# Optimization experiments

Measured on AMD Instinct MI355X. Metric: run time of the kernel, lower is better.

Reference implementation:

```python
import jax, jax.numpy as jnp
import numpy as np

B, N, E = 4, 50000, 800000
C_IN, C_OUT, K = 64, 64, 3  # K = max_degree
AVG_DEG = 16.0


def setup_inputs() -> dict:
    key = jax.random.key(0)
    k1, k2, k3, k4, k5 = jax.random.split(key, 5)
    x = jax.random.normal(k1, (B, N, C_IN), dtype=jnp.float32)
    lap_rows = jax.random.randint(k2, (E,), 0, N)
    lap_cols = jax.random.randint(k3, (E,), 0, N)
    # scale so ||L|| stays O(1) and the Chebyshev recursion is stable
    lap_vals = jax.random.normal(k4, (E,), dtype=jnp.float32) / AVG_DEG
    weights = jax.random.normal(k5, (K + 1, C_IN, C_OUT), dtype=jnp.float32) * 0.1
    bias = jnp.full((C_OUT,), 0.1, dtype=jnp.float32)
    return dict(x=x, lap_rows=lap_rows, lap_cols=lap_cols,
                lap_vals=lap_vals, weights=weights, bias=bias)


def reference(x, lap_rows, lap_cols, lap_vals, weights, bias):
    # Sparse L @ X via edge list: gather source rows, scale, scatter-add to dest rows.
    def spmm_one(xb):  # xb: [N, C]
        return jax.ops.segment_sum(lap_vals[:, None] * xb[lap_cols], lap_rows,
                                   num_segments=N)

    spmm = jax.vmap(spmm_one)  # [B, N, C] -> [B, N, C]

    Tx0 = x
    out = jnp.einsum('bnc,co->bno', Tx0, weights[0])
    Tx1 = spmm(Tx0)
    out = out + jnp.einsum('bnc,co->bno', Tx1, weights[1])
    for k in range(2, K + 1):
        Tx2 = 2.0 * spmm(Tx1) - Tx0
        out = out + jnp.einsum('bnc,co->bno', Tx2, weights[k])
        Tx0, Tx1 = Tx1, Tx2
    return jax.nn.relu(out + bias)
```

## Files before the change

### kernel.cpp

```cpp
#include <hip/hip_runtime.h>


#define N_NODES 50000
#define N_EDGES 800000
#define BATCH 4
#define CH 64
#define BN (N_NODES * CH)
#define ROWS_TOTAL (BATCH * N_NODES)
#define NB 782
#define EPB 4096
#define SCT_BLOCKS ((N_EDGES + EPB - 1) / EPB)

typedef unsigned int uint;
typedef unsigned short ushort;
typedef unsigned char uchar;
typedef __attribute__((ext_vector_type(8))) short short8;
typedef __attribute__((ext_vector_type(4))) float f32x4;

__device__ __forceinline__ uint pack_bf16(float lo, float hi) {
  uint a = __float_as_uint(lo);
  uint b = __float_as_uint(hi);
  a = (a + 0x7fffu + ((a >> 16) & 1u)) >> 16;
  b = (b + 0x7fffu + ((b >> 16) & 1u)) >> 16;
  return a | (b << 16);
}
__device__ __forceinline__ ushort bf16one(float x) {
  uint a = __float_as_uint(x);
  a = (a + 0x7fffu + ((a >> 16) & 1u)) >> 16;
  return (ushort)a;
}
__device__ __forceinline__ uint q_u8(float v, float inv) {
  return (uint)((int)rintf(v * inv) + 128) & 0xffu;
}

__global__ __launch_bounds__(1024) void bucket_hist(const int* __restrict__ rows,
                                                    int* __restrict__ gcounts) {
  __shared__ int h[NB];
  for (int b = threadIdx.x; b < NB; b += 1024) h[b] = 0;
  __syncthreads();
  int base_e = blockIdx.x * EPB;
#pragma unroll
  for (int j = 0; j < EPB / 1024; ++j) {
    int e = base_e + j * 1024 + threadIdx.x;
    if (e < N_EDGES) atomicAdd(&h[rows[e] >> 6], 1);
  }
  __syncthreads();
  for (int b = threadIdx.x; b < NB; b += 1024)
    if (h[b]) atomicAdd(&gcounts[b], h[b]);
}

__global__ __launch_bounds__(1024) void bucket_scan(const int* __restrict__ gcounts,
                                                    int* __restrict__ bucket_base,
                                                    int* __restrict__ gcursor) {
  __shared__ int s[1024];
  int t = threadIdx.x;
  int v = (t < NB) ? gcounts[t] : 0;
  s[t] = v;
  __syncthreads();
  for (int off = 1; off < 1024; off <<= 1) {
    int tv = (t >= off) ? s[t - off] : 0;
    __syncthreads();
    s[t] += tv;
    __syncthreads();
  }
  int ex = s[t] - v;
  if (t < NB) { bucket_base[t] = ex; gcursor[t] = ex; }
  if (t == NB) bucket_base[NB] = N_EDGES;
}

__global__ __launch_bounds__(1024) void bucket_scatter(const int* __restrict__ rows,
                                                       const int* __restrict__ cols,
                                                       const float* __restrict__ vals,
                                                       int* __restrict__ gcursor,
                                                       uint2* __restrict__ staging) {
  __shared__ int lcur[NB];
  for (int b = threadIdx.x; b < NB; b += 1024) lcur[b] = 0;
  __syncthreads();
  int base_e = blockIdx.x * EPB;
#pragma unroll
  for (int j = 0; j < EPB / 1024; ++j) {
    int e = base_e + j * 1024 + threadIdx.x;
    if (e < N_EDGES) atomicAdd(&lcur[rows[e] >> 6], 1);
  }
  __syncthreads();
  for (int b = threadIdx.x; b < NB; b += 1024) {
    int c = lcur[b];
    lcur[b] = (c > 0) ? atomicAdd(&gcursor[b], c) : 0;
  }
  __syncthreads();
#pragma unroll
  for (int j = 0; j < EPB / 1024; ++j) {
    int e = base_e + j * 1024 + threadIdx.x;
    if (e < N_EDGES) {
      int r = rows[e];
      int pos = atomicAdd(&lcur[r >> 6], 1);
      staging[pos] = make_uint2((uint)cols[e] | ((uint)(r & 63) << 20),
                                __float_as_uint(vals[e]));
    }
  }
}

__global__ __launch_bounds__(256) void bucket_finalize(const int* __restrict__ bucket_base,
                                                       const uint2* __restrict__ staging,
                                                       uint2* __restrict__ pairs,
                                                       int* __restrict__ row_start) {
  int b = blockIdx.x;
  int seg0 = bucket_base[b], seg1 = bucket_base[b + 1];
  __shared__ int hist[64];
  __shared__ int cur[64];
  if (threadIdx.x < 64) hist[threadIdx.x] = 0;
  __syncthreads();
  for (int i = seg0 + threadIdx.x; i < seg1; i += 256)
    atomicAdd(&hist[staging[i].x >> 20], 1);
  __syncthreads();
  if (threadIdx.x < 64) {
    int v = hist[threadIdx.x];
    int sc = v;
#pragma unroll
    for (int off = 1; off < 64; off <<= 1) {
      int t = __shfl_up(sc, off, 64);
      if (threadIdx.x >= (unsigned)off) sc += t;
    }
    int start = seg0 + sc - v;
    cur[threadIdx.x] = start;
    int r = b * 64 + threadIdx.x;
    if (r < N_NODES) row_start[r] = start;
    if (r == N_NODES) row_start[N_NODES] = N_EDGES;
  }
  __syncthreads();
  for (int i = seg0 + threadIdx.x; i < seg1; i += 256) {
    uint2 eu = staging[i];
    int rl = eu.x >> 20;
    int pos = atomicAdd(&cur[rl], 1);
    pairs[pos] = make_uint2(eu.x & 0xFFFFFu, eu.y);
  }
}

__global__ __launch_bounds__(256) void wprep_kernel(const float* __restrict__ w,
                                                    ushort* __restrict__ wtT) {
  int t = blockIdx.x * 256 + threadIdx.x;
  if (t >= 64 * 256) return;
  int o = t >> 8, k = t & 255, m = k >> 6, c = k & 63;
  int idx = c * 64 + o;
  float v;
  if (m == 0)      v = w[idx] - w[2 * 4096 + idx];
  else if (m == 1) v = w[4096 + idx] - 3.0f * w[3 * 4096 + idx];
  else if (m == 2) v = 2.0f * w[2 * 4096 + idx];
  else             v = 4.0f * w[3 * 4096 + idx];
  wtT[t] = bf16one(v);
}

__global__ __launch_bounds__(256) void cvt_kernel(const float* __restrict__ in,
                                                  uint* __restrict__ xu8w,
                                                  float* __restrict__ xsc) {
  int node = blockIdx.x * 4 + (threadIdx.x >> 6);
  int lane = threadIdx.x & 63;
  int b = lane >> 4;
  int c4 = (lane & 15) * 4;
  float4 v = *reinterpret_cast<const float4*>(in + (size_t)b * BN + (size_t)node * 64 + c4);
  float mx = fmaxf(fmaxf(fabsf(v.x), fabsf(v.y)), fmaxf(fabsf(v.z), fabsf(v.w)));
#pragma unroll
  for (int off = 1; off < 64; off <<= 1) mx = fmaxf(mx, __shfl_xor(mx, off, 64));
  float inv = mx > 0.f ? 127.0f / mx : 0.f;
  uint w8 = q_u8(v.x, inv) | (q_u8(v.y, inv) << 8) |
            (q_u8(v.z, inv) << 16) | (q_u8(v.w, inv) << 24);
  xu8w[(size_t)node * 64 + b * 16 + (lane & 15)] = w8;
  if (lane == 0) xsc[node] = mx * (1.0f / 127.0f);
}

__device__ __forceinline__ void fma16_u8(float acc[16], float& sm, float m,
                                         const uint4& w) {
  const uint arr[4] = {w.x, w.y, w.z, w.w};
#pragma unroll
  for (int t = 0; t < 4; ++t) {
    uint u = arr[t];
    acc[t * 4 + 0] = fmaf(m, (float)(u & 0xffu),         acc[t * 4 + 0]);
    acc[t * 4 + 1] = fmaf(m, (float)((u >> 8) & 0xffu),  acc[t * 4 + 1]);
    acc[t * 4 + 2] = fmaf(m, (float)((u >> 16) & 0xffu), acc[t * 4 + 2]);
    acc[t * 4 + 3] = fmaf(m, (float)(u >> 24),           acc[t * 4 + 3]);
  }
  sm += m;
}

__device__ __forceinline__ void spmm_body(const int* __restrict__ row_start,
                                          const uint2* __restrict__ pairs,
                                          const uchar* __restrict__ src,
                                          const float* __restrict__ ssc,
                                          uchar* __restrict__ dst,
                                          float* __restrict__ dsc) {
  int row = blockIdx.x * 4 + (threadIdx.x >> 6);
  int lane = threadIdx.x & 63;
  int q = lane >> 4;
  int ql = lane & 15;
  const uchar* sb = src + ql * 16;
  int s = row_start[row], e = row_start[row + 1];
  float acc[16];
  float sm = 0.f;
#pragma unroll
  for (int j = 0; j < 16; ++j) acc[j] = 0.f;
  int i = s;
  for (; i + 15 < e; i += 16) {
    uint2 p0 = pairs[i + q];
    uint2 p1 = pairs[i + 4 + q];
    uint2 p2 = pairs[i + 8 + q];
    uint2 p3 = pairs[i + 12 + q];
    uint4 q0 = *reinterpret_cast<const uint4*>(sb + (size_t)p0.x * 256);
    uint4 q1 = *reinterpret_cast<const uint4*>(sb + (size_t)p1.x * 256);
    uint4 q2 = *reinterpret_cast<const uint4*>(sb + (size_t)p2.x * 256);
    uint4 q3 = *reinterpret_cast<const uint4*>(sb + (size_t)p3.x * 256);
    float m0 = __uint_as_float(p0.y) * ssc[p0.x];
    float m1 = __uint_as_float(p1.y) * ssc[p1.x];
    float m2 = __uint_as_float(p2.y) * ssc[p2.x];
    float m3 = __uint_as_float(p3.y) * ssc[p3.x];
    fma16_u8(acc, sm, m0, q0);
    fma16_u8(acc, sm, m1, q1);
    fma16_u8(acc, sm, m2, q2);
    fma16_u8(acc, sm, m3, q3);
  }
  for (; i < e; i += 4) {
    if (i + q < e) {
      uint2 p0 = pairs[i + q];
      uint4 q0 = *reinterpret_cast<const uint4*>(sb + (size_t)p0.x * 256);
      fma16_u8(acc, sm, __uint_as_float(p0.y) * ssc[p0.x], q0);
    }
  }
#pragma unroll
  for (int j = 0; j < 16; ++j) {
    acc[j] += __shfl_xor(acc[j], 16, 64);
    acc[j] += __shfl_xor(acc[j], 32, 64);
  }
  sm += __shfl_xor(sm, 16, 64);
  sm += __shfl_xor(sm, 32, 64);
#pragma unroll
  for (int j = 0; j < 16; ++j) acc[j] = fmaf(-128.f, sm, acc[j]);
  float mx = 0.f;
#pragma unroll
  for (int j = 0; j < 16; ++j) mx = fmaxf(mx, fabsf(acc[j]));
#pragma unroll
  for (int off = 1; off < 16; off <<= 1) mx = fmaxf(mx, __shfl_xor(mx, off, 64));
  if (lane < 16) {
    float inv = mx > 0.f ? 127.0f / mx : 0.f;
    uint w[4];
#pragma unroll
    for (int t = 0; t < 4; ++t) {
      w[t] = q_u8(acc[t * 4 + 0], inv) | (q_u8(acc[t * 4 + 1], inv) << 8) |
             (q_u8(acc[t * 4 + 2], inv) << 16) | (q_u8(acc[t * 4 + 3], inv) << 24);
    }
    *reinterpret_cast<uint4*>(dst + (size_t)row * 256 + ql * 16) =
        make_uint4(w[0], w[1], w[2], w[3]);
    if (lane == 0) dsc[row] = mx * (1.0f / 127.0f);
  }
}

__global__ __launch_bounds__(256) void spmm_s1(const int* __restrict__ rs,
                                               const uint2* __restrict__ pr,
                                               const uchar* __restrict__ src,
                                               const float* __restrict__ ssc,
                                               uchar* __restrict__ dst,
                                               float* __restrict__ dsc) {
  spmm_body(rs, pr, src, ssc, dst, dsc);
}
__global__ __launch_bounds__(256) void spmm_s2(const int* __restrict__ rs,
                                               const uint2* __restrict__ pr,
                                               const uchar* __restrict__ src,
                                               const float* __restrict__ ssc,
                                               uchar* __restrict__ dst,
                                               float* __restrict__ dsc) {
  spmm_body(rs, pr, src, ssc, dst, dsc);
}
__global__ __launch_bounds__(256) void spmm_s3(const int* __restrict__ rs,
                                               const uint2* __restrict__ pr,
                                               const uchar* __restrict__ src,
                                               const float* __restrict__ ssc,
                                               uchar* __restrict__ dst,
                                               float* __restrict__ dsc) {
  spmm_body(rs, pr, src, ssc, dst, dsc);
}

__device__ __forceinline__ short8 dequant8_u8(uint2 q, float sc, float nb) {
  float f0 = fmaf((float)(q.x & 0xffu),         sc, nb);
  float f1 = fmaf((float)((q.x >> 8) & 0xffu),  sc, nb);
  float f2 = fmaf((float)((q.x >> 16) & 0xffu), sc, nb);
  float f3 = fmaf((float)(q.x >> 24),           sc, nb);
  float f4 = fmaf((float)(q.y & 0xffu),         sc, nb);
  float f5 = fmaf((float)((q.y >> 8) & 0xffu),  sc, nb);
  float f6 = fmaf((float)((q.y >> 16) & 0xffu), sc, nb);
  float f7 = fmaf((float)(q.y >> 24),           sc, nb);
  uint4 v = make_uint4(pack_bf16(f0, f1), pack_bf16(f2, f3),
                       pack_bf16(f4, f5), pack_bf16(f6, f7));
  return __builtin_bit_cast(short8, v);
}

__global__ __launch_bounds__(256) void gemm4_mfma(
    const uchar* __restrict__ A0u8, const float* __restrict__ A0sc,
    const uchar* __restrict__ A1u8, const float* __restrict__ A1sc,
    const uchar* __restrict__ A2u8, const float* __restrict__ A2sc,
    const uchar* __restrict__ A3u8, const float* __restrict__ A3sc,
    const uint* __restrict__ wtT,
    const float* __restrict__ bias, float* __restrict__ out) {
  __shared__ uint WS[64 * 132];
  __shared__ float bias_s[64];
  for (int w = threadIdx.x; w < 8192; w += 256)
    WS[(w >> 7) * 132 + (w & 127)] = wtT[w];
  if (threadIdx.x < 64) bias_s[threadIdx.x] = bias[threadIdx.x];
  __syncthreads();

  const int lane = threadIdx.x & 63;
  const int wv = threadIdx.x >> 6;
  const int r0 = blockIdx.x * 64 + wv * 16;
  const int c16 = lane & 15;
  const int hi = lane >> 4;

  const int ar = r0 + c16;
  const size_t arow_b = (size_t)ar * 64 + hi * 8;
  const int nd = ar >> 2;
  const float sc0 = A0sc[nd];
  const float sc1 = A1sc[nd];
  const float sc2 = A2sc[nd];
  const float sc3 = A3sc[nd];

  f32x4 acc[4] = {{0.f, 0.f, 0.f, 0.f}, {0.f, 0.f, 0.f, 0.f},
                  {0.f, 0.f, 0.f, 0.f}, {0.f, 0.f, 0.f, 0.f}};

#pragma unroll
  for (int ks = 0; ks < 8; ++ks) {
    const int m = ks >> 1;
    const uchar* Au = (m == 0) ? A0u8 : (m == 1) ? A1u8 : (m == 2) ? A2u8 : A3u8;
    const float sc = (m == 0) ? sc0 : (m == 1) ? sc1 : (m == 2) ? sc2 : sc3;
    uint2 qv = *reinterpret_cast<const uint2*>(Au + arow_b + (ks & 1) * 32);
    short8 afrag = dequant8_u8(qv, sc, -128.f * sc);
#pragma unroll
    for (int nt = 0; nt < 4; ++nt) {
      uint4 bv = *reinterpret_cast<const uint4*>(
          &WS[(nt * 16 + c16) * 132 + ks * 16 + hi * 4]);
      short8 bfrag = __builtin_bit_cast(short8, bv);
      acc[nt] = __builtin_amdgcn_mfma_f32_16x16x32_bf16(afrag, bfrag, acc[nt], 0, 0, 0);
    }
  }

#pragma unroll
  for (int nt = 0; nt < 4; ++nt) {
#pragma unroll
    for (int i = 0; i < 4; ++i) {
      int row = r0 + hi * 4 + i;
      int node = row >> 2, b = row & 3;
      int col = nt * 16 + c16;
      float v = acc[nt][i] + bias_s[col];
      out[(size_t)b * BN + (size_t)node * 64 + col] = fmaxf(v, 0.f);
    }
  }
}

extern "C" void kernel_launch(void* const* d_in, const int* in_sizes, int n_in,
                              void* d_out, int out_size, void* d_ws, size_t ws_size,
                              hipStream_t stream) {
  const float* x        = (const float*)d_in[0];
  const int*   lap_rows = (const int*)d_in[1];
  const int*   lap_cols = (const int*)d_in[2];
  const float* lap_vals = (const float*)d_in[3];
  const float* weights  = (const float*)d_in[4];
  const float* bias     = (const float*)d_in[5];
  float* out = (float*)d_out;

  char* ws = (char*)d_ws;
  size_t off = 0;
  auto alloc = [&](size_t bytes) {
    void* p = ws + off;
    off += (bytes + 255) & ~(size_t)255;
    return p;
  };
  int*    gcounts     = (int*)alloc((size_t)NB * 4);
  int*    gcursor     = (int*)alloc((size_t)NB * 4);
  int*    bucket_base = (int*)alloc((size_t)(NB + 1) * 4);
  int*    row_start   = (int*)alloc((size_t)(N_NODES + 1) * 4);
  uint2*  pairs       = (uint2*)alloc((size_t)N_EDGES * 8);
  uint2*  staging     = (uint2*)alloc((size_t)N_EDGES * 8);
  ushort* wtT         = (ushort*)alloc((size_t)64 * 256 * 2);
  uchar*  xu8         = (uchar*)alloc((size_t)N_NODES * 256);
  uchar*  S1u         = (uchar*)alloc((size_t)N_NODES * 256);
  uchar*  S2u         = (uchar*)alloc((size_t)N_NODES * 256);
  uchar*  S3u         = (uchar*)alloc((size_t)N_NODES * 256);
  float*  xsc         = (float*)alloc((size_t)N_NODES * 4);
  float*  S1sc        = (float*)alloc((size_t)N_NODES * 4);
  float*  S2sc        = (float*)alloc((size_t)N_NODES * 4);
  float*  S3sc        = (float*)alloc((size_t)N_NODES * 4);
  (void)ws_size; (void)in_sizes; (void)n_in; (void)out_size;

  wprep_kernel<<<64, 256, 0, stream>>>(weights, wtT);
  cvt_kernel<<<N_NODES / 4, 256, 0, stream>>>(x, (uint*)xu8, xsc);
  hipMemsetAsync(gcounts, 0, (size_t)NB * 4, stream);
  bucket_hist<<<SCT_BLOCKS, 1024, 0, stream>>>(lap_rows, gcounts);
  bucket_scan<<<1, 1024, 0, stream>>>(gcounts, bucket_base, gcursor);
  bucket_scatter<<<SCT_BLOCKS, 1024, 0, stream>>>(lap_rows, lap_cols, lap_vals,
                                                  gcursor, staging);
  bucket_finalize<<<NB, 256, 0, stream>>>(bucket_base, staging, pairs, row_start);

  const int spmm_blocks = N_NODES / 4;

  spmm_s1<<<spmm_blocks, 256, 0, stream>>>(row_start, pairs, xu8, xsc, S1u, S1sc);
  spmm_s2<<<spmm_blocks, 256, 0, stream>>>(row_start, pairs, S1u, S1sc, S2u, S2sc);
  spmm_s3<<<spmm_blocks, 256, 0, stream>>>(row_start, pairs, S2u, S2sc, S3u, S3sc);
  gemm4_mfma<<<ROWS_TOTAL / 64, 256, 0, stream>>>(xu8, xsc, S1u, S1sc, S2u, S2sc,
                                                  S3u, S3sc, (const uint*)wtT,
                                                  bias, out);
}
```

Measured before the change: 218.1 us.

## Replace global atomic bucket cursors with per-block count matrix and scan; shorten SpMM unroll

The bucket sort now has each histogram block write its per-bucket counts to a bucket-major count matrix. A single-block scan produces a per-(bucket, block) base offset, so the scatter kernel no longer recounts edges or takes global atomic cursors. This also drops the memset. Edges per block are doubled (fewer blocks), and the SpMM inner loop is unrolled over 8 edges instead of 16, which lowers register pressure but leaves fewer loads in flight. The single-block scan over about 78K entries is serial per thread and may cost more than the old 782-entry scan.

```diff
diff --git a/kernel.cpp b/kernel.cpp
--- a/kernel.cpp
+++ b/kernel.cpp
@@ -8,8 +8,9 @@
 #define BN (N_NODES * CH)
 #define ROWS_TOTAL (BATCH * N_NODES)
 #define NB 782
-#define EPB 4096
+#define EPB 8192
 #define SCT_BLOCKS ((N_EDGES + EPB - 1) / EPB)
+#define TOTC (NB * SCT_BLOCKS)
 
 typedef unsigned int uint;
 typedef unsigned short ushort;
@@ -34,7 +35,7 @@
 }
 
 __global__ __launch_bounds__(1024) void bucket_hist(const int* __restrict__ rows,
-                                                    int* __restrict__ gcounts) {
+                                                    int* __restrict__ bcounts) {
   __shared__ int h[NB];
   for (int b = threadIdx.x; b < NB; b += 1024) h[b] = 0;
   __syncthreads();
@@ -46,48 +47,43 @@
   }
   __syncthreads();
   for (int b = threadIdx.x; b < NB; b += 1024)
-    if (h[b]) atomicAdd(&gcounts[b], h[b]);
-}
-
-__global__ __launch_bounds__(1024) void bucket_scan(const int* __restrict__ gcounts,
-                                                    int* __restrict__ bucket_base,
-                                                    int* __restrict__ gcursor) {
-  __shared__ int s[1024];
-  int t = threadIdx.x;
-  int v = (t < NB) ? gcounts[t] : 0;
-  s[t] = v;
+    bcounts[(size_t)b * SCT_BLOCKS + blockIdx.x] = h[b];
+}
+
+__global__ __launch_bounds__(1024) void scan2_kernel(const int* __restrict__ bc,
+                                                     int* __restrict__ bases) {
+  __shared__ int sums[1024];
+  int tid = threadIdx.x;
+  const int per = (TOTC + 1023) / 1024;
+  int begin = tid * per;
+  int end = begin + per; if (end > TOTC) end = TOTC;
+  int s = 0;
+  for (int i = begin; i < end; ++i) s += bc[i];
+  sums[tid] = s;
   __syncthreads();
   for (int off = 1; off < 1024; off <<= 1) {
-    int tv = (t >= off) ? s[t - off] : 0;
+    int t = (tid >= off) ? sums[tid - off] : 0;
     __syncthreads();
-    s[t] += tv;
+    sums[tid] += t;
     __syncthreads();
   }
-  int ex = s[t] - v;
-  if (t < NB) { bucket_base[t] = ex; gcursor[t] = ex; }
-  if (t == NB) bucket_base[NB] = N_EDGES;
+  int running = sums[tid] - s;
+  for (int i = begin; i < end; ++i) {
+    bases[i] = running;
+    running += bc[i];
+  }
 }
 
 __global__ __launch_bounds__(1024) void bucket_scatter(const int* __restrict__ rows,
                                                        const int* __restrict__ cols,
                                                        const float* __restrict__ vals,
-                                                       int* __restrict__ gcursor,
+                                                       const int* __restrict__ bases,
                                                        uint2* __restrict__ staging) {
   __shared__ int lcur[NB];
-  for (int b = threadIdx.x; b < NB; b += 1024) lcur[b] = 0;
+  for (int b = threadIdx.x; b < NB; b += 1024)
+    lcur[b] = bases[(size_t)b * SCT_BLOCKS + blockIdx.x];
   __syncthreads();
   int base_e = blockIdx.x * EPB;
-#pragma unroll
-  for (int j = 0; j < EPB / 1024; ++j) {
-    int e = base_e + j * 1024 + threadIdx.x;
-    if (e < N_EDGES) atomicAdd(&lcur[rows[e] >> 6], 1);
-  }
-  __syncthreads();
-  for (int b = threadIdx.x; b < NB; b += 1024) {
-    int c = lcur[b];
-    lcur[b] = (c > 0) ? atomicAdd(&gcursor[b], c) : 0;
-  }
-  __syncthreads();
 #pragma unroll
   for (int j = 0; j < EPB / 1024; ++j) {
     int e = base_e + j * 1024 + threadIdx.x;
@@ -100,12 +96,13 @@
   }
 }
 
-__global__ __launch_bounds__(256) void bucket_finalize(const int* __restrict__ bucket_base,
+__global__ __launch_bounds__(256) void bucket_finalize(const int* __restrict__ bases,
                                                        const uint2* __restrict__ staging,
                                                        uint2* __restrict__ pairs,
                                                        int* __restrict__ row_start) {
   int b = blockIdx.x;
-  int seg0 = bucket_base[b], seg1 = bucket_base[b + 1];
+  int seg0 = bases[(size_t)b * SCT_BLOCKS];
+  int seg1 = (b == NB - 1) ? N_EDGES : bases[(size_t)(b + 1) * SCT_BLOCKS];
   __shared__ int hist[64];
   __shared__ int cur[64];
   if (threadIdx.x < 64) hist[threadIdx.x] = 0;
@@ -199,23 +196,15 @@
 #pragma unroll
   for (int j = 0; j < 16; ++j) acc[j] = 0.f;
   int i = s;
-  for (; i + 15 < e; i += 16) {
-    uint2 p0 = pairs[i + q];
-    uint2 p1 = pairs[i + 4 + q];
-    uint2 p2 = pairs[i + 8 + q];
-    uint2 p3 = pairs[i + 12 + q];
-    uint4 q0 = *reinterpret_cast<const uint4*>(sb + (size_t)p0.x * 256);
-    uint4 q1 = *reinterpret_cast<const uint4*>(sb + (size_t)p1.x * 256);
-    uint4 q2 = *reinterpret_cast<const uint4*>(sb + (size_t)p2.x * 256);
-    uint4 q3 = *reinterpret_cast<const uint4*>(sb + (size_t)p3.x * 256);
-    float m0 = __uint_as_float(p0.y) * ssc[p0.x];
-    float m1 = __uint_as_float(p1.y) * ssc[p1.x];
-    float m2 = __uint_as_float(p2.y) * ssc[p2.x];
-    float m3 = __uint_as_float(p3.y) * ssc[p3.x];
-    fma16_u8(acc, sm, m0, q0);
-    fma16_u8(acc, sm, m1, q1);
-    fma16_u8(acc, sm, m2, q2);
-    fma16_u8(acc, sm, m3, q3);
+  for (; i + 7 < e; i += 8) {
+    uint2 pa = pairs[i + q];
+    uint2 pb = pairs[i + 4 + q];
+    uint4 qa = *reinterpret_cast<const uint4*>(sb + (size_t)pa.x * 256);
+    uint4 qb = *reinterpret_cast<const uint4*>(sb + (size_t)pb.x * 256);
+    float ma = __uint_as_float(pa.y) * ssc[pa.x];
+    float mb = __uint_as_float(pb.y) * ssc[pb.x];
+    fma16_u8(acc, sm, ma, qa);
+    fma16_u8(acc, sm, mb, qb);
   }
   for (; i < e; i += 4) {
     if (i + q < e) {
@@ -369,9 +358,8 @@
     off += (bytes + 255) & ~(size_t)255;
     return p;
   };
-  int*    gcounts     = (int*)alloc((size_t)NB * 4);
-  int*    gcursor     = (int*)alloc((size_t)NB * 4);
-  int*    bucket_base = (int*)alloc((size_t)(NB + 1) * 4);
+  int*    bcounts     = (int*)alloc((size_t)TOTC * 4);
+  int*    bases       = (int*)alloc((size_t)TOTC * 4);
   int*    row_start   = (int*)alloc((size_t)(N_NODES + 1) * 4);
   uint2*  pairs       = (uint2*)alloc((size_t)N_EDGES * 8);
   uint2*  staging     = (uint2*)alloc((size_t)N_EDGES * 8);
@@ -388,12 +376,11 @@
 
   wprep_kernel<<<64, 256, 0, stream>>>(weights, wtT);
   cvt_kernel<<<N_NODES / 4, 256, 0, stream>>>(x, (uint*)xu8, xsc);
-  hipMemsetAsync(gcounts, 0, (size_t)NB * 4, stream);
-  bucket_hist<<<SCT_BLOCKS, 1024, 0, stream>>>(lap_rows, gcounts);
-  bucket_scan<<<1, 1024, 0, stream>>>(gcounts, bucket_base, gcursor);
+  bucket_hist<<<SCT_BLOCKS, 1024, 0, stream>>>(lap_rows, bcounts);
+  scan2_kernel<<<1, 1024, 0, stream>>>(bcounts, bases);
   bucket_scatter<<<SCT_BLOCKS, 1024, 0, stream>>>(lap_rows, lap_cols, lap_vals,
-                                                  gcursor, staging);
-  bucket_finalize<<<NB, 256, 0, stream>>>(bucket_base, staging, pairs, row_start);
+                                                  bases, staging);
+  bucket_finalize<<<NB, 256, 0, stream>>>(bases, staging, pairs, row_start);
 
   const int spmm_blocks = N_NODES / 4;
 
```

New measurement: 300.9 us. +38.0%, slower.
